# Performance work log

Measured on AMD Instinct MI355X. Metric: run time of the kernel, lower is better.

## Reference

```python
import jax, jax.numpy as jnp
import numpy as np

B, N, D, H = 4, 2048, 768, 12
DH = D // H  # 64


def setup_inputs() -> dict:
    key = jax.random.key(0)
    k1, k2, k3 = jax.random.split(key, 3)
    x = jax.random.normal(k1, (B, N, D), dtype=jnp.float32)
    # causal mask, broadcastable over (b, h): 1 = keep, 0 = masked
    mask = jnp.tril(jnp.ones((N, N), dtype=jnp.int32))[None, None, :, :]
    w_qkv = jax.random.normal(k2, (D, 3 * D), dtype=jnp.float32) * 0.02
    w_out = jax.random.normal(k3, (D, D), dtype=jnp.float32) * 0.02
    return {"x": x, "mask": mask, "w_qkv": w_qkv, "w_out": w_out}


def reference(x, mask, w_qkv, w_out):
    b, n, d = x.shape
    qkv = x @ w_qkv                               # [b, n, 3d]
    q, k, v = jnp.split(qkv, 3, axis=-1)
    def to_heads(t):
        return t.reshape(b, n, H, DH).transpose(0, 2, 1, 3)  # [b, h, n, dh]
    q, k, v = to_heads(q), to_heads(k), to_heads(v)
    attn = jnp.einsum('bhqd,bhkd->bhqk', q, k) / jnp.sqrt(jnp.float32(DH))
    attn = jnp.where(mask == 0, -jnp.inf, attn)
    attn = jax.nn.softmax(attn.astype(jnp.float32), axis=-1).astype(x.dtype)
    out = jnp.einsum('bhqk,bhkd->bhqd', attn, v)  # [b, h, n, dh]
    out = out.transpose(0, 2, 1, 3).reshape(b, n, d)
    return out @ w_out
```

## Files before the change

kernel.cpp:

```cpp
#include <hip/hip_runtime.h>
#include <stdint.h>

#define B_  4
#define N_  2048
#define D_  768
#define H_  12
#define DH_ 64
#define TD  (3*D_)
#define M_  (B_*N_)

typedef __bf16 bf16x8 __attribute__((ext_vector_type(8)));
typedef float  f32x4  __attribute__((ext_vector_type(4)));
typedef unsigned int   u32x4 __attribute__((ext_vector_type(4)));
typedef unsigned short u16x4 __attribute__((ext_vector_type(4)));

__device__ __forceinline__ unsigned short f2bf(float f) {
  union { float f; uint32_t u; } c; c.f = f;
  uint32_t u = c.u;
  uint32_t r = (u + 0x7FFFu + ((u >> 16) & 1u)) >> 16;
  return (unsigned short)r;
}

__device__ __forceinline__ void gload16(const unsigned short* g, unsigned short* l) {
  __builtin_amdgcn_global_load_lds(
      (const __attribute__((address_space(1))) void*)g,
      (__attribute__((address_space(3))) void*)l, 16, 0, 0);
}

__global__ __launch_bounds__(256)
void convx_kernel(const float* __restrict__ x, unsigned short* __restrict__ xb) {
  int i = (blockIdx.x * 256 + threadIdx.x) * 8;
  f32x4 a = *(const f32x4*)(x + i);
  f32x4 b = *(const f32x4*)(x + i + 4);
  u16x4 lo, hi;
  lo.x = f2bf(a.x); lo.y = f2bf(a.y); lo.z = f2bf(a.z); lo.w = f2bf(a.w);
  hi.x = f2bf(b.x); hi.y = f2bf(b.y); hi.z = f2bf(b.z); hi.w = f2bf(b.w);
  *(u16x4*)(xb + i) = lo;
  *(u16x4*)(xb + i + 4) = hi;
}

__global__ __launch_bounds__(256)
void convwT_kernel(const float* __restrict__ W, unsigned short* __restrict__ WT,
                   int R, int C, float sc, int qcols) {
  __shared__ float tile[32][33];
  const int C0 = blockIdx.x * 32, R0 = blockIdx.y * 32;
  const int t = threadIdx.x;
  {
    int r = t >> 3, c4 = (t & 7) * 4;
    f32x4 v = *(const f32x4*)(W + (size_t)(R0 + r) * C + C0 + c4);
    tile[r][c4] = v.x; tile[r][c4 + 1] = v.y; tile[r][c4 + 2] = v.z; tile[r][c4 + 3] = v.w;
  }
  __syncthreads();
  {
    int n = t >> 3, r4 = (t & 7) * 4;
    float s = (C0 + n) < qcols ? sc : 1.0f;
    u16x4 o;
    o.x = f2bf(tile[r4][n] * s);
    o.y = f2bf(tile[r4 + 1][n] * s);
    o.z = f2bf(tile[r4 + 2][n] * s);
    o.w = f2bf(tile[r4 + 3][n] * s);
    *(u16x4*)(WT + (size_t)(C0 + n) * R + R0 + r4) = o;
  }
}

template <bool OUT_BF16>
__global__ __launch_bounds__(256)
void gemm_bt_kernel(const unsigned short* __restrict__ A,
                    const unsigned short* __restrict__ BT,
                    void* __restrict__ Cv, int M, int N, int K) {
  __shared__ unsigned short As[128 * 64];
  __shared__ unsigned short Bs[128 * 64];
  const int tid  = threadIdx.x;
  const int lane = tid & 63;
  const int wave = tid >> 6;
  const int wr = wave >> 1, wc = wave & 1;
  const int l15 = lane & 15, lh = lane >> 4;
  const int row0 = blockIdx.y * 128;
  const int col0 = blockIdx.x * 128;

  const unsigned short* ga[4];
  const unsigned short* gb[4];
  unsigned short* la = As + wave * 2048;
  unsigned short* lb = Bs + wave * 2048;
  #pragma unroll
  for (int q = 0; q < 4; ++q) {
    int rl = 32 * wave + 8 * q + (lane >> 3);
    int kb = (((lane & 7) << 4) ^ ((rl & 7) << 4)) >> 1;
    ga[q] = A  + (size_t)(row0 + rl) * K + kb;
    gb[q] = BT + (size_t)(col0 + rl) * K + kb;
  }

  f32x4 acc[4][4] = {};

  for (int k0 = 0; k0 < K; k0 += 64) {
    #pragma unroll
    for (int q = 0; q < 4; ++q) {
      gload16(ga[q], la + q * 512);
      gload16(gb[q], lb + q * 512);
      ga[q] += 64; gb[q] += 64;
    }
    __syncthreads();

    #pragma unroll
    for (int ks = 0; ks < 2; ++ks) {
      bf16x8 af[4], bfv[4];
      #pragma unroll
      for (int mf = 0; mf < 4; ++mf) {
        int r = wr * 64 + mf * 16 + l15;
        af[mf] = *(const bf16x8*)((const char*)As +
                  ((r * 128 + ks * 64 + lh * 16) ^ ((r & 7) << 4)));
      }
      #pragma unroll
      for (int nf = 0; nf < 4; ++nf) {
        int n = wc * 64 + nf * 16 + l15;
        bfv[nf] = *(const bf16x8*)((const char*)Bs +
                  ((n * 128 + ks * 64 + lh * 16) ^ ((n & 7) << 4)));
      }
      __builtin_amdgcn_s_setprio(1);
      #pragma unroll
      for (int mf = 0; mf < 4; ++mf)
        #pragma unroll
        for (int nf = 0; nf < 4; ++nf)
          acc[mf][nf] = __builtin_amdgcn_mfma_f32_16x16x32_bf16(af[mf], bfv[nf], acc[mf][nf], 0, 0, 0);
      __builtin_amdgcn_s_setprio(0);
    }
    __syncthreads();
  }

  #pragma unroll
  for (int mf = 0; mf < 4; ++mf) {
    #pragma unroll
    for (int nf = 0; nf < 4; ++nf) {
      #pragma unroll
      for (int rg = 0; rg < 4; ++rg) {
        int rr = row0 + wr * 64 + mf * 16 + lh * 4 + rg;
        int cc = col0 + wc * 64 + nf * 16 + l15;
        float v = acc[mf][nf][rg];
        if constexpr (OUT_BF16) ((unsigned short*)Cv)[(size_t)rr * N + cc] = f2bf(v);
        else                    ((float*)Cv)[(size_t)rr * N + cc] = v;
      }
    }
  }
}

__global__ __launch_bounds__(256)
void attn_kernel(const unsigned short* __restrict__ qkv,
                 float* __restrict__ Oacc, float* __restrict__ Lacc) {
  __shared__ unsigned short Ks[2][64 * 64];
  __shared__ unsigned short Vs[2][64 * 64];
  __shared__ unsigned short Ps[4 * 32 * 64];
  const int tid  = threadIdx.x;
  const int lane = tid & 63, wave = tid >> 6;
  const int l15 = lane & 15, lh = lane >> 4;

  const int g = blockIdx.x;
  const int j = g >> 3;
  const int bh = (j / 40) * 8 + (g & 7);
  const int r = j % 40;
  const int b = bh / H_, h = bh % H_;
  const short cum[17] = {0,1,2,3,4,6,8,10,12,15,18,21,24,28,32,36,40};
  int qb = 15;
  #pragma unroll
  for (int q = 15; q > 0; --q) if (r < cum[q]) qb = q - 1;
  const int chunk = r - cum[qb];
  const int t0 = chunk * 8;
  const int t1 = min(t0 + 8, 2 * (qb + 1));
  const int q0 = qb * 128 + wave * 32;

  bf16x8 qf[2][2];
  #pragma unroll
  for (int mf = 0; mf < 2; ++mf)
    #pragma unroll
    for (int ks = 0; ks < 2; ++ks)
      qf[mf][ks] = *(const bf16x8*)(qkv + (size_t)(b * N_ + q0 + mf * 16 + l15) * TD
                                    + h * DH_ + ks * 32 + lh * 8);

  f32x4 o[2][4] = {};
  float ls[2][4] = {};

  u32x4 kr[2], vr[2];
  const int s_kv = tid >> 3, s_d8 = tid & 7;

  auto ISSUE = [&](int t) {
    #pragma unroll
    for (int it = 0; it < 2; ++it) {
      int kv = s_kv + it * 32;
      size_t base = (size_t)(b * N_ + t * 64 + kv) * TD + h * DH_ + s_d8 * 8;
      kr[it] = *(const u32x4*)(qkv + base + D_);
      vr[it] = *(const u32x4*)(qkv + base + 2 * D_);
    }
  };
  auto WRITE = [&](int buf) {
    #pragma unroll
    for (int it = 0; it < 2; ++it) {
      int kv = s_kv + it * 32;
      *(u32x4*)(&Ks[buf][kv * 64 + ((s_d8 * 8) ^ ((kv & 7) << 3))]) = kr[it];
      const unsigned short* vsp = (const unsigned short*)&vr[it];
      #pragma unroll
      for (int jj = 0; jj < 8; ++jj) {
        int d = s_d8 * 8 + jj;
        int swz = (jj ^ s_d8) & 7;
        Vs[buf][d * 64 + (kv ^ (swz << 3))] = vsp[jj];
      }
    }
  };

  ISSUE(t0); WRITE(0); __syncthreads();

  for (int t = t0; t < t1; ++t) {
    const int cur = (t - t0) & 1;
    const bool more = (t + 1 < t1);
    if (more) ISSUE(t + 1);

    const int kv0 = t * 64;
    if (kv0 <= q0 + 31) {
      f32x4 s[2][4] = {};
      __builtin_amdgcn_s_setprio(1);
      #pragma unroll
      for (int ks = 0; ks < 2; ++ks) {
        bf16x8 kf[4];
        #pragma unroll
        for (int nf = 0; nf < 4; ++nf) {
          int kv = nf * 16 + l15;
          kf[nf] = *(const bf16x8*)(&Ks[cur][kv * 64 + ((ks * 32 + lh * 8) ^ ((kv & 7) << 3))]);
        }
        #pragma unroll
        for (int mf = 0; mf < 2; ++mf)
          #pragma unroll
          for (int nf = 0; nf < 4; ++nf)
            s[mf][nf] = __builtin_amdgcn_mfma_f32_16x16x32_bf16(qf[mf][ks], kf[nf], s[mf][nf], 0, 0, 0);
      }
      __builtin_amdgcn_s_setprio(0);

      const bool need_mask = (kv0 + 63 > q0);
      #pragma unroll
      for (int mf = 0; mf < 2; ++mf) {
        #pragma unroll
        for (int rg = 0; rg < 4; ++rg) {
          const int row = q0 + mf * 16 + lh * 4 + rg;
          const int prow = mf * 16 + lh * 4 + rg;
          float lacc = 0.f;
          #pragma unroll
          for (int nf = 0; nf < 4; ++nf) {
            int col = kv0 + nf * 16 + l15;
            float p = exp2f(s[mf][nf][rg]);
            if (need_mask && col > row) p = 0.f;
            lacc += p;
            Ps[wave * 2048 + prow * 64 + ((nf * 16 + l15) ^ ((prow & 7) << 3))] = f2bf(p);
          }
          ls[mf][rg] += lacc;
        }
      }

      __builtin_amdgcn_s_setprio(1);
      #pragma unroll
      for (int ks = 0; ks < 2; ++ks) {
        bf16x8 pf[2], vf[4];
        #pragma unroll
        for (int mf = 0; mf < 2; ++mf) {
          int pr = mf * 16 + l15;
          pf[mf] = *(const bf16x8*)(&Ps[wave * 2048 + pr * 64 + ((ks * 32 + lh * 8) ^ ((pr & 7) << 3))]);
        }
        #pragma unroll
        for (int nf = 0; nf < 4; ++nf) {
          int d = nf * 16 + l15;
          int swz = ((d & 7) ^ ((d >> 3) & 7)) & 7;
          vf[nf] = *(const bf16x8*)(&Vs[cur][d * 64 + ((ks * 32 + lh * 8) ^ (swz << 3))]);
        }
        #pragma unroll
        for (int mf = 0; mf < 2; ++mf)
          #pragma unroll
          for (int nf = 0; nf < 4; ++nf)
            o[mf][nf] = __builtin_amdgcn_mfma_f32_16x16x32_bf16(pf[mf], vf[nf], o[mf][nf], 0, 0, 0);
      }
      __builtin_amdgcn_s_setprio(0);
    }

    if (more) WRITE(cur ^ 1);
    __syncthreads();
  }

  #pragma unroll
  for (int mf = 0; mf < 2; ++mf)
    #pragma unroll
    for (int rg = 0; rg < 4; ++rg) {
      float v = ls[mf][rg];
      v += __shfl_xor(v, 1); v += __shfl_xor(v, 2);
      v += __shfl_xor(v, 4); v += __shfl_xor(v, 8);
      ls[mf][rg] = v;
    }
  if (l15 == 0) {
    #pragma unroll
    for (int rg = 0; rg < 4; ++rg)
      atomicAdd(&Lacc[(size_t)(b * N_ + q0 + lh * 4 + rg) * H_ + h], ls[0][rg]);
  } else if (l15 == 8) {
    #pragma unroll
    for (int rg = 0; rg < 4; ++rg)
      atomicAdd(&Lacc[(size_t)(b * N_ + q0 + 16 + lh * 4 + rg) * H_ + h], ls[1][rg]);
  }
  #pragma unroll
  for (int mf = 0; mf < 2; ++mf)
    #pragma unroll
    for (int rg = 0; rg < 4; ++rg) {
      int row = q0 + mf * 16 + lh * 4 + rg;
      #pragma unroll
      for (int nf = 0; nf < 4; ++nf)
        atomicAdd(&Oacc[(size_t)(b * N_ + row) * D_ + h * DH_ + nf * 16 + l15], o[mf][nf][rg]);
    }
}

__global__ __launch_bounds__(256)
void norm_kernel(const float* __restrict__ Oacc, const float* __restrict__ Lacc,
                 unsigned short* __restrict__ ctx) {
  int e8 = blockIdx.x * 256 + threadIdx.x;
  int row = e8 / 96, c8 = e8 % 96;
  int h = c8 >> 3;
  float inv = 1.f / Lacc[(size_t)row * H_ + h];
  const float* src = Oacc + (size_t)row * D_ + c8 * 8;
  f32x4 a = *(const f32x4*)(src);
  f32x4 bb = *(const f32x4*)(src + 4);
  u16x4 lo, hi;
  lo.x = f2bf(a.x * inv); lo.y = f2bf(a.y * inv); lo.z = f2bf(a.z * inv); lo.w = f2bf(a.w * inv);
  hi.x = f2bf(bb.x * inv); hi.y = f2bf(bb.y * inv); hi.z = f2bf(bb.z * inv); hi.w = f2bf(bb.w * inv);
  unsigned short* dst = ctx + (size_t)row * D_ + c8 * 8;
  *(u16x4*)(dst) = lo;
  *(u16x4*)(dst + 4) = hi;
}

extern "C" void kernel_launch(void* const* d_in, const int* in_sizes, int n_in,
                              void* d_out, int out_size, void* d_ws, size_t ws_size,
                              hipStream_t stream) {
  const float* x     = (const float*)d_in[0];
  const float* w_qkv = (const float*)d_in[2];
  const float* w_out = (const float*)d_in[3];

  char* ws = (char*)d_ws;
  unsigned short* qkv = (unsigned short*)ws;
  unsigned short* ctx = (unsigned short*)(ws + 37748736);
  float* Lacc         = (float*)(ws + 50331648);
  unsigned short* wTq = (unsigned short*)(ws + 50724864);
  unsigned short* wTo = (unsigned short*)(ws + 54263808);
  unsigned short* x_bf = (unsigned short*)d_out;
  float* Oacc = (float*)d_out;
  float* out  = (float*)d_out;

  const float SC = 0.18033688011112042f;
  dim3 blk(256);

  convx_kernel<<<dim3(M_ * D_ / 2048), blk, 0, stream>>>(x, x_bf);
  convwT_kernel<<<dim3(TD / 32, D_ / 32), blk, 0, stream>>>(w_qkv, wTq, D_, TD, SC, D_);
  convwT_kernel<<<dim3(D_ / 32, D_ / 32), blk, 0, stream>>>(w_out, wTo, D_, D_, 1.0f, 0);
  hipMemsetAsync(Lacc, 0, 393216, stream);
  gemm_bt_kernel<true><<<dim3(TD / 128, M_ / 128), blk, 0, stream>>>(x_bf, wTq, qkv, M_, TD, D_);
  hipMemsetAsync(Oacc, 0, 25165824, stream);
  attn_kernel<<<dim3(48 * 40), blk, 0, stream>>>(qkv, Oacc, Lacc);
  norm_kernel<<<dim3(M_ * 96 / 256), blk, 0, stream>>>(Oacc, Lacc, ctx);
  gemm_bt_kernel<false><<<dim3(D_ / 128, M_ / 128), blk, 0, stream>>>(ctx, wTo, out, M_, D_, D_);
}
```

Before: 290.8 us.

## Add XCD-aware block remap, narrower out-proj tile, coalesced LDS loads

The GEMM kernel now takes a 1D grid and remaps block IDs round-robin across the 8 XCDs, so neighbouring tiles share L2. Global-to-LDS loads are reorganised so each wave fills contiguous rows across the whole block. The output projection uses a 128x64 tile to launch more workgroups on the small N=768 GEMM. The bf16 conversion now uses the native __bf16 cast instead of manual rounding. The remap assumes the grid size is divisible by 8, and the narrower tile reuses each loaded A tile across fewer output columns.

```diff
diff --git a/kernel.cpp b/kernel.cpp
--- a/kernel.cpp
+++ b/kernel.cpp
@@ -15,10 +15,8 @@
 typedef unsigned short u16x4 __attribute__((ext_vector_type(4)));
 
 __device__ __forceinline__ unsigned short f2bf(float f) {
-  union { float f; uint32_t u; } c; c.f = f;
-  uint32_t u = c.u;
-  uint32_t r = (u + 0x7FFFu + ((u >> 16) & 1u)) >> 16;
-  return (unsigned short)r;
+  __bf16 h = (__bf16)f;
+  return *(unsigned short*)&h;
 }
 
 __device__ __forceinline__ void gload16(const unsigned short* g, unsigned short* l) {
@@ -63,47 +61,52 @@
   }
 }
 
-template <bool OUT_BF16>
+template <bool OUT_BF16, int BN>
 __global__ __launch_bounds__(256)
 void gemm_bt_kernel(const unsigned short* __restrict__ A,
                     const unsigned short* __restrict__ BT,
                     void* __restrict__ Cv, int M, int N, int K) {
   __shared__ unsigned short As[128 * 64];
-  __shared__ unsigned short Bs[128 * 64];
+  __shared__ unsigned short Bs[BN * 64];
+  constexpr int QB = BN / 32;
+  constexpr int NF = BN / 32;
   const int tid  = threadIdx.x;
   const int lane = tid & 63;
   const int wave = tid >> 6;
   const int wr = wave >> 1, wc = wave & 1;
   const int l15 = lane & 15, lh = lane >> 4;
-  const int row0 = blockIdx.y * 128;
-  const int col0 = blockIdx.x * 128;
-
+
+  const int nwg = gridDim.x;
+  const int bid = blockIdx.x;
+  const int nb  = (bid & 7) * (nwg >> 3) + (bid >> 3);
+  const int nbx = N / BN;
+  const int row0 = (nb / nbx) * 128;
+  const int col0 = (nb % nbx) * BN;
+
+  const int kb = (((tid & 7) ^ ((tid >> 3) & 7)) << 3);
   const unsigned short* ga[4];
-  const unsigned short* gb[4];
-  unsigned short* la = As + wave * 2048;
-  unsigned short* lb = Bs + wave * 2048;
-  #pragma unroll
-  for (int q = 0; q < 4; ++q) {
-    int rl = 32 * wave + 8 * q + (lane >> 3);
-    int kb = (((lane & 7) << 4) ^ ((rl & 7) << 4)) >> 1;
-    ga[q] = A  + (size_t)(row0 + rl) * K + kb;
-    gb[q] = BT + (size_t)(col0 + rl) * K + kb;
-  }
-
-  f32x4 acc[4][4] = {};
+  const unsigned short* gb[QB];
+  unsigned short* lA = As + wave * 512;
+  unsigned short* lB = Bs + wave * 512;
+  #pragma unroll
+  for (int q = 0; q < 4; ++q)
+    ga[q] = A + (size_t)(row0 + q * 32 + (tid >> 3)) * K + kb;
+  #pragma unroll
+  for (int q = 0; q < QB; ++q)
+    gb[q] = BT + (size_t)(col0 + q * 32 + (tid >> 3)) * K + kb;
+
+  f32x4 acc[4][NF] = {};
 
   for (int k0 = 0; k0 < K; k0 += 64) {
     #pragma unroll
-    for (int q = 0; q < 4; ++q) {
-      gload16(ga[q], la + q * 512);
-      gload16(gb[q], lb + q * 512);
-      ga[q] += 64; gb[q] += 64;
-    }
+    for (int q = 0; q < 4; ++q) { gload16(ga[q], lA + q * 2048); ga[q] += 64; }
+    #pragma unroll
+    for (int q = 0; q < QB; ++q) { gload16(gb[q], lB + q * 2048); gb[q] += 64; }
     __syncthreads();
 
     #pragma unroll
     for (int ks = 0; ks < 2; ++ks) {
-      bf16x8 af[4], bfv[4];
+      bf16x8 af[4], bfv[NF];
       #pragma unroll
       for (int mf = 0; mf < 4; ++mf) {
         int r = wr * 64 + mf * 16 + l15;
@@ -111,8 +114,8 @@
                   ((r * 128 + ks * 64 + lh * 16) ^ ((r & 7) << 4)));
       }
       #pragma unroll
-      for (int nf = 0; nf < 4; ++nf) {
-        int n = wc * 64 + nf * 16 + l15;
+      for (int nf = 0; nf < NF; ++nf) {
+        int n = wc * (BN / 2) + nf * 16 + l15;
         bfv[nf] = *(const bf16x8*)((const char*)Bs +
                   ((n * 128 + ks * 64 + lh * 16) ^ ((n & 7) << 4)));
       }
@@ -120,7 +123,7 @@
       #pragma unroll
       for (int mf = 0; mf < 4; ++mf)
         #pragma unroll
-        for (int nf = 0; nf < 4; ++nf)
+        for (int nf = 0; nf < NF; ++nf)
           acc[mf][nf] = __builtin_amdgcn_mfma_f32_16x16x32_bf16(af[mf], bfv[nf], acc[mf][nf], 0, 0, 0);
       __builtin_amdgcn_s_setprio(0);
     }
@@ -130,11 +133,11 @@
   #pragma unroll
   for (int mf = 0; mf < 4; ++mf) {
     #pragma unroll
-    for (int nf = 0; nf < 4; ++nf) {
+    for (int nf = 0; nf < NF; ++nf) {
       #pragma unroll
       for (int rg = 0; rg < 4; ++rg) {
         int rr = row0 + wr * 64 + mf * 16 + lh * 4 + rg;
-        int cc = col0 + wc * 64 + nf * 16 + l15;
+        int cc = col0 + wc * (BN / 2) + nf * 16 + l15;
         float v = acc[mf][nf][rg];
         if constexpr (OUT_BF16) ((unsigned short*)Cv)[(size_t)rr * N + cc] = f2bf(v);
         else                    ((float*)Cv)[(size_t)rr * N + cc] = v;
@@ -351,9 +354,11 @@
   convwT_kernel<<<dim3(TD / 32, D_ / 32), blk, 0, stream>>>(w_qkv, wTq, D_, TD, SC, D_);
   convwT_kernel<<<dim3(D_ / 32, D_ / 32), blk, 0, stream>>>(w_out, wTo, D_, D_, 1.0f, 0);
   hipMemsetAsync(Lacc, 0, 393216, stream);
-  gemm_bt_kernel<true><<<dim3(TD / 128, M_ / 128), blk, 0, stream>>>(x_bf, wTq, qkv, M_, TD, D_);
+  gemm_bt_kernel<true, 128><<<dim3((TD / 128) * (M_ / 128)), blk, 0, stream>>>(
+      x_bf, wTq, qkv, M_, TD, D_);
   hipMemsetAsync(Oacc, 0, 25165824, stream);
   attn_kernel<<<dim3(48 * 40), blk, 0, stream>>>(qkv, Oacc, Lacc);
   norm_kernel<<<dim3(M_ * 96 / 256), blk, 0, stream>>>(Oacc, Lacc, ctx);
-  gemm_bt_kernel<false><<<dim3(D_ / 128, M_ / 128), blk, 0, stream>>>(ctx, wTo, out, M_, D_, D_);
-}
+  gemm_bt_kernel<false, 64><<<dim3((D_ / 64) * (M_ / 128)), blk, 0, stream>>>(
+      ctx, wTo, out, M_, D_, D_);
+}
```

New measurement: 285.8 us. Within noise of the previous version (-1.7%).
